# Performance work log

Measured on AMD Instinct MI355X. Metric: run time of the kernel, lower is better.

Reference implementation:

```python
import jax, jax.numpy as jnp
import numpy as np

NF, IN_NF, N_LAYERS = 64, 196, 3
B, H, W = 1, 256, 256
P3 = [(1, 1), (1, 1)]
P1 = [(0, 0), (0, 0)]


def conv2d(x, w, pad):
    return jax.lax.conv_general_dilated(x, w, (1, 1), pad,
                                        dimension_numbers=('NCHW', 'OIHW', 'NCHW'))


def prelu(x, a):
    return jnp.where(x >= 0, x, a[None, :, None, None] * x)


def warp(x, flow):
    # standard backward bilinear warp, zero padding outside the image
    Bx, C, Hx, Wx = x.shape
    yy, xx = jnp.meshgrid(jnp.arange(Hx, dtype=x.dtype),
                          jnp.arange(Wx, dtype=x.dtype), indexing='ij')
    px = xx[None] + flow[:, 0]  # (B,H,W)
    py = yy[None] + flow[:, 1]

    def sample(img, px, py):  # img (C,H,W); px,py (H,W)
        x0 = jnp.floor(px)
        y0 = jnp.floor(py)
        x1 = x0 + 1.0
        y1 = y0 + 1.0
        wx1 = px - x0
        wx0 = 1.0 - wx1
        wy1 = py - y0
        wy0 = 1.0 - wy1

        def gather(xi, yi):
            valid = (xi >= 0) & (xi <= Wx - 1) & (yi >= 0) & (yi <= Hx - 1)
            xc = jnp.clip(xi, 0, Wx - 1).astype(jnp.int32)
            yc = jnp.clip(yi, 0, Hx - 1).astype(jnp.int32)
            return img[:, yc, xc] * valid.astype(img.dtype)

        return (gather(x0, y0) * (wx0 * wy0) + gather(x1, y0) * (wx1 * wy0)
                + gather(x0, y1) * (wx0 * wy1) + gather(x1, y1) * (wx1 * wy1))

    return jax.vmap(sample)(x, px, py)


def setup_inputs() -> dict:
    key = jax.random.key(0)
    ks = jax.random.split(key, 11)
    s = 0.05
    return {
        'feat_0': jax.random.normal(ks[0], (B, 64, H, W), jnp.float32),
        'feat_1': jax.random.normal(ks[1], (B, 64, H, W), jnp.float32),
        'feat_dense': jax.random.normal(ks[2], (B, 64, H, W), jnp.float32),
        'flow': jax.random.normal(ks[3], (B, 4, H, W), jnp.float32),
        'space_mask': jax.random.uniform(ks[4], (B, 1, H, W), jnp.float32),
        'head_w': jax.random.normal(ks[5], (IN_NF, IN_NF, 3, 3), jnp.float32) * s,
        'head_a': jnp.full((IN_NF,), 0.25, jnp.float32),
        'conv_w': jax.random.normal(ks[6], (N_LAYERS, IN_NF, IN_NF, 3, 3), jnp.float32) * s,
        'conv_a': jnp.full((N_LAYERS, IN_NF), 0.25, jnp.float32),
        'last_w': jax.random.normal(ks[7], (4 + NF, IN_NF * (N_LAYERS + 1), 1, 1), jnp.float32) * s,
        'last_b': jax.random.normal(ks[8], (4 + NF,), jnp.float32) * s,
        'mask_w': jax.random.normal(ks[9], (2, NF, 3, 3), jnp.float32) * s,
        'mask_b': jax.random.normal(ks[10], (2,), jnp.float32) * s,
    }


def reference(feat_0, feat_1, feat_dense, flow, space_mask,
              head_w, head_a, conv_w, conv_a, last_w, last_b, mask_w, mask_b):
    f0 = warp(feat_0, flow[:, :2])
    f1 = warp(feat_1, flow[:, 2:4])
    x = jnp.concatenate([f0, f1, feat_dense, flow], axis=1)  # (B, in_nf, H, W)
    sm_up = jnp.repeat(jnp.repeat(space_mask, 2, axis=2), 2, axis=3)

    # head: conv3x3 -> PReLU, then mask (dense / use_sparsity=False path)
    x = prelu(conv2d(x, head_w, P3), head_a) * space_mask
    outs = [x]
    for i in range(N_LAYERS):
        x = conv2d(x, conv_w[i], P3) * space_mask
        x = prelu(x, conv_a[i])
        outs.append(x)
    x = conv2d(jnp.concatenate(outs, axis=1), last_w, P1) + last_b[None, :, None, None]

    smn = conv2d(x[:, 4:], mask_w, P3) + mask_b[None, :, None, None]

    Bx, Cx, Hx, Wx = x.shape
    x_up = jax.image.resize(x, (Bx, Cx, 2 * Hx, 2 * Wx), method='bilinear')
    smn_up = jax.image.resize(smn, (Bx, 2, 2 * Hx, 2 * Wx), method='bilinear')

    flow_out = x_up[:, :4]
    feat_t = x_up[:, 4:]
    # eval-mode mask (training=False): hard argmax between channel 0 and 1
    mask_next = (smn_up[:, :1] > smn_up[:, 1:2]).astype(x.dtype) * sm_up
    return flow_out, feat_t, mask_next
```

## Files before the change

kernel.cpp:

```cpp
#include <hip/hip_runtime.h>

typedef _Float16 f16;
typedef _Float16 f16x8 __attribute__((ext_vector_type(8)));
typedef _Float16 f16x4 __attribute__((ext_vector_type(4)));
typedef float    f32x4 __attribute__((ext_vector_type(4)));

#define MFMA16(a,b,c) __builtin_amdgcn_mfma_f32_16x16x32_f16(a,b,c,0,0,0)

#define NPIX 65536
#define CSTR 448
#define RB   (256*CSTR*2)
#define SBUF ((size_t)258*256*CSTR*2)

#define PK_OB   1024
#define PK_CB   14336
#define PK_TAP  100352
#define PK_CONV 903168
#define PKL_CB  5120
#define PKL_BI  35840

#define STG_BYTES 17408

__global__ void k_pack_conv(const float* __restrict__ head_w,
                            const float* __restrict__ conv_w,
                            f16* __restrict__ dst)
{
    int t = blockIdx.x*256 + threadIdx.x;
    if (t >= 4*9*7*14*2*64) return;
    int lane = t & 63; t >>= 6;
    int sel  = t & 1;  t >>= 1;
    int ob   = t % 14; t /= 14;
    int cb   = t % 7;  t /= 7;
    int tap  = t % 9;  t /= 9;
    int li   = t;
    const float* W = (li == 0) ? head_w : (conv_w + (size_t)(li-1)*196*196*9);
    int oc  = ob*16 + (lane & 15);
    int ic0 = cb*32 + (lane >> 4)*8;
    f16x8 v;
#pragma unroll
    for (int j = 0; j < 8; ++j) {
        int ic = ic0 + j;
        float x = 0.f;
        if (oc < 196 && ic < 196) x = W[((size_t)oc*196 + ic)*9 + tap];
        f16 h = (f16)x;
        v[j] = (sel == 0) ? h : (f16)(x - (float)h);
    }
    *(f16x8*)(dst + (size_t)li*PK_CONV +
              (((size_t)((tap*7+cb)*14 + ob)*2 + sel)*64 + lane)*8) = v;
}

__global__ void k_pack_last(const float* __restrict__ last_w, f16* __restrict__ dst)
{
    int t = blockIdx.x*256 + threadIdx.x;
    if (t >= 4*7*5*2*64) return;
    int lane = t & 63; t >>= 6;
    int sel  = t & 1;  t >>= 1;
    int ob   = t % 5;  t /= 5;
    int cb   = t % 7;  t /= 7;
    int bi   = t;
    int oc = ob*16 + (lane & 15);
    int k0 = cb*32 + (lane >> 4)*8;
    f16x8 v;
#pragma unroll
    for (int j = 0; j < 8; ++j) {
        int k = k0 + j;
        float x = 0.f;
        if (oc < 68 && k < 196) x = last_w[(size_t)oc*784 + bi*196 + k];
        f16 h = (f16)x;
        v[j] = (sel == 0) ? h : (f16)(x - (float)h);
    }
    *(f16x8*)(dst + (((size_t)((bi*7+cb)*5 + ob)*2 + sel)*64 + lane)*8) = v;
}

struct Gath { int o00,o01,o10,o11; float w00,w01,w10,w11; };

__device__ inline Gath mk_gath(float pxf, float pyf)
{
    float x0 = floorf(pxf), y0 = floorf(pyf);
    float x1 = x0 + 1.f, y1 = y0 + 1.f;
    float wx1 = pxf - x0, wx0 = 1.f - wx1;
    float wy1 = pyf - y0, wy0 = 1.f - wy1;
    bool vx0 = (x0 >= 0.f) && (x0 <= 255.f);
    bool vx1 = (x1 >= 0.f) && (x1 <= 255.f);
    bool vy0 = (y0 >= 0.f) && (y0 <= 255.f);
    bool vy1 = (y1 >= 0.f) && (y1 <= 255.f);
    int ix0 = min(max((int)x0, 0), 255);
    int ix1 = min(max((int)x1, 0), 255);
    int iy0 = min(max((int)y0, 0), 255);
    int iy1 = min(max((int)y1, 0), 255);
    Gath g;
    g.o00 = iy0*256 + ix0; g.w00 = (vx0 && vy0) ? wx0*wy0 : 0.f;
    g.o01 = iy0*256 + ix1; g.w01 = (vx1 && vy0) ? wx1*wy0 : 0.f;
    g.o10 = iy1*256 + ix0; g.w10 = (vx0 && vy1) ? wx0*wy1 : 0.f;
    g.o11 = iy1*256 + ix1; g.w11 = (vx1 && vy1) ? wx1*wy1 : 0.f;
    return g;
}

__device__ inline void store4(f16* __restrict__ op, int c0,
                              float a, float b, float c, float d)
{
    f16x4 hi, lo;
    f16 h;
    h = (f16)a; hi[0] = h; lo[0] = (f16)(a - (float)h);
    h = (f16)b; hi[1] = h; lo[1] = (f16)(b - (float)h);
    h = (f16)c; hi[2] = h; lo[2] = (f16)(c - (float)h);
    h = (f16)d; hi[3] = h; lo[3] = (f16)(d - (float)h);
    f16* p = op + (c0 >> 5)*64 + (c0 & 31);
    *(f16x4*)p        = hi;
    *(f16x4*)(p + 32) = lo;
}

__global__ void k_warp_concat(const float* __restrict__ f0, const float* __restrict__ f1,
                              const float* __restrict__ fd, const float* __restrict__ flow,
                              f16* __restrict__ out)
{
    int px = blockIdx.x*256 + threadIdx.x;
    int row = px >> 8, col = px & 255;
    f16* op = out + ((size_t)(row+1)*256 + col)*CSTR;
    Gath g0 = mk_gath((float)col + flow[px],          (float)row + flow[NPIX   + px]);
    Gath g1 = mk_gath((float)col + flow[2*NPIX + px], (float)row + flow[3*NPIX + px]);
#pragma unroll
    for (int c = 0; c < 64; c += 4) {
        float v[4];
#pragma unroll
        for (int r = 0; r < 4; ++r) {
            const float* im = f0 + (size_t)(c+r)*NPIX;
            v[r] = g0.w00*im[g0.o00] + g0.w01*im[g0.o01] + g0.w10*im[g0.o10] + g0.w11*im[g0.o11];
        }
        store4(op, c, v[0], v[1], v[2], v[3]);
    }
#pragma unroll
    for (int c = 0; c < 64; c += 4) {
        float v[4];
#pragma unroll
        for (int r = 0; r < 4; ++r) {
            const float* im = f1 + (size_t)(c+r)*NPIX;
            v[r] = g1.w00*im[g1.o00] + g1.w01*im[g1.o01] + g1.w10*im[g1.o10] + g1.w11*im[g1.o11];
        }
        store4(op, 64 + c, v[0], v[1], v[2], v[3]);
    }
#pragma unroll
    for (int c = 0; c < 64; c += 4) {
        store4(op, 128 + c, fd[(size_t)(c+0)*NPIX + px], fd[(size_t)(c+1)*NPIX + px],
                            fd[(size_t)(c+2)*NPIX + px], fd[(size_t)(c+3)*NPIX + px]);
    }
    store4(op, 192, flow[px], flow[NPIX+px], flow[2*NPIX+px], flow[3*NPIX+px]);
#pragma unroll
    for (int c = 196; c < 224; c += 4) store4(op, c, 0.f, 0.f, 0.f, 0.f);
}

__global__ __launch_bounds__(512, 4)
void k_conv3x3(const f16* __restrict__ in, f16* __restrict__ out,
               const f16* __restrict__ pack, const float* __restrict__ alpha,
               const float* __restrict__ mask, const f16* __restrict__ zp)
{
    __shared__ __align__(16) char bs[2*STG_BYTES];

    int bid = blockIdx.x;
    int wg  = (bid & 7)*64 + (bid >> 3);
    int row  = wg >> 1;
    int col0 = (wg & 1) << 7;

    int tid  = threadIdx.x;
    int lane = tid & 63;
    int w    = tid >> 6;
    int l15  = lane & 15, lk = lane >> 4;
    int och7   = (w & 1)*7;
    int pxbase = (w >> 1)*32;

    f32x4 acc[7][2];
#pragma unroll
    for (int o = 0; o < 7; ++o)
#pragma unroll
        for (int pb = 0; pb < 2; ++pb)
            acc[o][pb] = (f32x4){0.f,0.f,0.f,0.f};

    auto stage = [&](char* bufn, int ky, int cb) {
#pragma unroll
        for (int u = 0; u < 3; ++u) {
            int j = u*8 + w;
            if (j < 17) {
                int p  = j*8 + (lane >> 3);
                int sl = lane & 7;
                int cp = col0 - 1 + p;
                const f16* src;
                if (p < 130 && (unsigned)cp < 256u)
                    src = in + ((size_t)(row+ky)*256 + cp)*CSTR + cb*64 + ((sl ^ (p & 7)) * 8);
                else
                    src = zp + lane*8;
                __builtin_amdgcn_global_load_lds(
                    (const __attribute__((address_space(1))) void*)src,
                    (__attribute__((address_space(3))) void*)(bufn + j*1024),
                    16, 0, 0);
            }
        }
    };

    stage(bs, 0, 0);
    __syncthreads();

    for (int idx = 0; idx < 21; ++idx) {
        int ky = idx / 7;
        int cb = idx - ky*7;
        int nidx = idx + 1;
        if (nidx < 21) {
            int nky = nidx / 7;
            stage(bs + (nidx & 1)*STG_BYTES, nky, nidx - nky*7);
        }

        const char* bufc = bs + (idx & 1)*STG_BYTES;
        __builtin_amdgcn_s_setprio(1);
#pragma unroll
        for (int kx = 0; kx < 3; ++kx) {
            const f16* ap = pack + ((size_t)(((ky*3+kx)*7 + cb)*14 + och7))*1024 + (size_t)lane*8;
            f16x8 bh[2], bl[2];
#pragma unroll
            for (int pb = 0; pb < 2; ++pb) {
                int t = pxbase + pb*16 + l15 + kx;
                int sz = t & 7;
                const char* base = bufc + t*128;
                bh[pb] = *(const f16x8*)(base + ((lk ^ sz) << 4));
                bl[pb] = *(const f16x8*)(base + (((4+lk) ^ sz) << 4));
            }
#pragma unroll
            for (int o = 0; o < 7; ++o) {
                f16x8 ah = *(const f16x8*)(ap + o*1024);
                f16x8 al = *(const f16x8*)(ap + o*1024 + 512);
#pragma unroll
                for (int pb = 0; pb < 2; ++pb) {
                    acc[o][pb] = MFMA16(ah, bh[pb], acc[o][pb]);
                    acc[o][pb] = MFMA16(ah, bl[pb], acc[o][pb]);
                    acc[o][pb] = MFMA16(al, bh[pb], acc[o][pb]);
                }
            }
        }
        __builtin_amdgcn_s_setprio(0);
        __syncthreads();
    }

    float mv[2];
#pragma unroll
    for (int pb = 0; pb < 2; ++pb) mv[pb] = mask[row*256 + col0 + pxbase + pb*16 + l15];
#pragma unroll
    for (int o = 0; o < 7; ++o) {
        int oc0 = och7*16 + o*16 + lk*4;
        f32x4 a4 = *(const f32x4*)(alpha + min(oc0, 192));
#pragma unroll
        for (int pb = 0; pb < 2; ++pb) {
            f32x4 d = acc[o][pb];
            f16x4 hi, lo;
#pragma unroll
            for (int r = 0; r < 4; ++r) {
                float v = d[r];
                v = (v >= 0.f ? v : a4[r]*v) * mv[pb];
                f16 h = (f16)v;
                hi[r] = h;
                lo[r] = (f16)(v - (float)h);
            }
            f16* op = out + ((size_t)(row+1)*256 + col0 + pxbase + pb*16 + l15)*CSTR
                          + (oc0 >> 5)*64 + (oc0 & 31);
            *(f16x4*)op        = hi;
            *(f16x4*)(op + 32) = lo;
        }
    }
}

__global__ __launch_bounds__(256, 4)
void k_acc_last(const f16* __restrict__ in, const f16* __restrict__ pack,
                const float* __restrict__ bias, float* __restrict__ accp, int bi)
{
    int lane = threadIdx.x & 63;
    int wid  = (blockIdx.x << 2) | (threadIdx.x >> 6);
    int row  = wid >> 3;
    int col0 = (wid & 7) << 5;
    int l15 = lane & 15, lk = lane >> 4;

    f32x4 acc[5][2];
#pragma unroll
    for (int i = 0; i < 5; ++i)
#pragma unroll
        for (int j = 0; j < 2; ++j)
            acc[i][j] = (f32x4){0.f, 0.f, 0.f, 0.f};

    const f16* bb = in + ((size_t)(row+1)*256 + col0 + l15)*CSTR + lk*8;
    const f16* ap = pack + (size_t)bi*PKL_BI + (size_t)lane*8;
    for (int cb = 0; cb < 7; ++cb) {
        f16x8 bh[2], bl[2];
#pragma unroll
        for (int pb = 0; pb < 2; ++pb) {
            const f16* p = bb + (size_t)pb*(16*CSTR) + cb*64;
            bh[pb] = *(const f16x8*)p;
            bl[pb] = *(const f16x8*)(p + 32);
        }
        const f16* a = ap + cb*PKL_CB;
#pragma unroll
        for (int ob = 0; ob < 5; ++ob) {
            f16x8 ah = *(const f16x8*)(a + ob*1024);
            f16x8 al = *(const f16x8*)(a + ob*1024 + 512);
#pragma unroll
            for (int pb = 0; pb < 2; ++pb) {
                acc[ob][pb] = MFMA16(ah, bh[pb], acc[ob][pb]);
                acc[ob][pb] = MFMA16(ah, bl[pb], acc[ob][pb]);
                acc[ob][pb] = MFMA16(al, bh[pb], acc[ob][pb]);
            }
        }
    }
#pragma unroll
    for (int ob = 0; ob < 5; ++ob) {
        int oc0 = ob*16 + lk*4;
#pragma unroll
        for (int pb = 0; pb < 2; ++pb) {
            int px = row*256 + col0 + pb*16 + l15;
            float* dst = accp + (size_t)px*80 + oc0;
            f32x4 d = acc[ob][pb];
            if (bi == 0) {
                f32x4 b4;
#pragma unroll
                for (int r = 0; r < 4; ++r) b4[r] = bias[min(oc0 + r, 67)];
                *(f32x4*)dst = d + b4;
            } else {
                *(f32x4*)dst = *(const f32x4*)dst + d;
            }
        }
    }
}

__global__ void k_smn(const float* __restrict__ accp, const float* __restrict__ mw,
                      const float* __restrict__ mb, float* __restrict__ smn)
{
    int px = blockIdx.x*256 + threadIdx.x;
    int row = px >> 8, col = px & 255;
    float s0 = mb[0], s1 = mb[1];
    for (int ky = 0; ky < 3; ++ky) {
        int r = row + ky - 1;
        if ((unsigned)r > 255u) continue;
        for (int kx = 0; kx < 3; ++kx) {
            int c = col + kx - 1;
            if ((unsigned)c > 255u) continue;
            const float* ab = accp + ((size_t)r*256 + c)*80 + 4;
            const float* w  = mw + ky*3 + kx;
#pragma unroll
            for (int ch = 0; ch < 64; ch += 4) {
                f32x4 v = *(const f32x4*)(ab + ch);
                s0 += v[0]*w[(ch+0)*9] + v[1]*w[(ch+1)*9] + v[2]*w[(ch+2)*9] + v[3]*w[(ch+3)*9];
                s1 += v[0]*w[(64+ch+0)*9] + v[1]*w[(64+ch+1)*9] + v[2]*w[(64+ch+2)*9] + v[3]*w[(64+ch+3)*9];
            }
        }
    }
    smn[px]        = s0;
    smn[NPIX + px] = s1;
}

__global__ void k_upsample(const float* __restrict__ accp, float* __restrict__ outp)
{
    int o = blockIdx.x*256 + threadIdx.x;
    int oy = o >> 9, ox = o & 511;
    int my = oy >> 1, mx = ox >> 1;
    int r0, r1, c0, c1; float wy0, wy1, wx0, wx1;
    if (oy & 1) { r0 = my;            r1 = min(my+1, 255); wy0 = 0.75f; wy1 = 0.25f; }
    else        { r0 = max(my-1, 0);  r1 = my;             wy0 = 0.25f; wy1 = 0.75f; }
    if (ox & 1) { c0 = mx;            c1 = min(mx+1, 255); wx0 = 0.75f; wx1 = 0.25f; }
    else        { c0 = max(mx-1, 0);  c1 = mx;             wx0 = 0.25f; wx1 = 0.75f; }
    const float* p00 = accp + ((size_t)r0*256 + c0)*80;
    const float* p01 = accp + ((size_t)r0*256 + c1)*80;
    const float* p10 = accp + ((size_t)r1*256 + c0)*80;
    const float* p11 = accp + ((size_t)r1*256 + c1)*80;
    float w00 = wy0*wx0, w01 = wy0*wx1, w10 = wy1*wx0, w11 = wy1*wx1;
#pragma unroll
    for (int ch = 0; ch < 68; ch += 4) {
        f32x4 va = *(const f32x4*)(p00 + ch);
        f32x4 vb = *(const f32x4*)(p01 + ch);
        f32x4 vc = *(const f32x4*)(p10 + ch);
        f32x4 vd = *(const f32x4*)(p11 + ch);
        f32x4 v;
#pragma unroll
        for (int r = 0; r < 4; ++r)
            v[r] = w00*va[r] + w01*vb[r] + w10*vc[r] + w11*vd[r];
        outp[(size_t)(ch+0)*262144 + o] = v[0];
        outp[(size_t)(ch+1)*262144 + o] = v[1];
        outp[(size_t)(ch+2)*262144 + o] = v[2];
        outp[(size_t)(ch+3)*262144 + o] = v[3];
    }
}

__global__ void k_mask(const float* __restrict__ smn, const float* __restrict__ sm,
                       float* __restrict__ outp)
{
    int o = blockIdx.x*256 + threadIdx.x;
    int oy = o >> 9, ox = o & 511;
    int my = oy >> 1, mx = ox >> 1;
    int r0, r1, c0, c1; float wy0, wy1, wx0, wx1;
    if (oy & 1) { r0 = my;            r1 = min(my+1, 255); wy0 = 0.75f; wy1 = 0.25f; }
    else        { r0 = max(my-1, 0);  r1 = my;             wy0 = 0.25f; wy1 = 0.75f; }
    if (ox & 1) { c0 = mx;            c1 = min(mx+1, 255); wx0 = 0.75f; wx1 = 0.25f; }
    else        { c0 = max(mx-1, 0);  c1 = mx;             wx0 = 0.25f; wx1 = 0.75f; }
    float w00 = wy0*wx0, w01 = wy0*wx1, w10 = wy1*wx0, w11 = wy1*wx1;
    int i00 = r0*256 + c0, i01 = r0*256 + c1, i10 = r1*256 + c0, i11 = r1*256 + c1;
    float s0 = w00*smn[i00] + w01*smn[i01] + w10*smn[i10] + w11*smn[i11];
    float s1 = w00*smn[NPIX+i00] + w01*smn[NPIX+i01] + w10*smn[NPIX+i10] + w11*smn[NPIX+i11];
    outp[(size_t)68*262144 + o] = (s0 > s1) ? sm[my*256 + mx] : 0.f;
}

extern "C" void kernel_launch(void* const* d_in, const int* in_sizes, int n_in,
                              void* d_out, int out_size, void* d_ws, size_t ws_size,
                              hipStream_t stream)
{
    const float* feat0  = (const float*)d_in[0];
    const float* feat1  = (const float*)d_in[1];
    const float* featd  = (const float*)d_in[2];
    const float* flow   = (const float*)d_in[3];
    const float* smask  = (const float*)d_in[4];
    const float* head_w = (const float*)d_in[5];
    const float* head_a = (const float*)d_in[6];
    const float* conv_w = (const float*)d_in[7];
    const float* conv_a = (const float*)d_in[8];
    const float* last_w = (const float*)d_in[9];
    const float* last_b = (const float*)d_in[10];
    const float* mask_w = (const float*)d_in[11];
    const float* mask_b = (const float*)d_in[12];
    float* outp = (float*)d_out;

    char* ws = (char*)d_ws;
    size_t off = 0;
    f16* zp = (f16*)(ws + off); off += 4096;
    f16* bufA = (f16*)(ws + off); off += SBUF + 4096;
    f16* bufB = (f16*)(ws + off); off += SBUF + 4096;
    f16* packc = (f16*)(ws + off); off += (size_t)4*PK_CONV*2;
    f16* packl = (f16*)(ws + off); off += (size_t)4*PKL_BI*2;
    float* accp = (float*)(ws + off); off += (size_t)NPIX*80*4;
    float* smn  = (float*)(ws + off); off += (size_t)2*NPIX*4;

    hipMemsetAsync(zp, 0, 4096, stream);
    hipMemsetAsync(bufA, 0, RB, stream);
    hipMemsetAsync((char*)bufA + (size_t)257*RB, 0, RB, stream);
    hipMemsetAsync(bufB, 0, RB, stream);
    hipMemsetAsync((char*)bufB + (size_t)257*RB, 0, RB, stream);

    k_pack_conv<<<1764, 256, 0, stream>>>(head_w, conv_w, packc);
    k_pack_last<<<70, 256, 0, stream>>>(last_w, packl);
    k_warp_concat<<<256, 256, 0, stream>>>(feat0, feat1, featd, flow, bufA);

    k_conv3x3<<<512, 512, 0, stream>>>(bufA, bufB, packc, head_a, smask, zp);
    k_acc_last<<<512, 256, 0, stream>>>(bufB, packl, last_b, accp, 0);
    k_conv3x3<<<512, 512, 0, stream>>>(bufB, bufA, packc + (size_t)1*PK_CONV, conv_a, smask, zp);
    k_acc_last<<<512, 256, 0, stream>>>(bufA, packl, last_b, accp, 1);
    k_conv3x3<<<512, 512, 0, stream>>>(bufA, bufB, packc + (size_t)2*PK_CONV, conv_a + 196, smask, zp);
    k_acc_last<<<512, 256, 0, stream>>>(bufB, packl, last_b, accp, 2);
    k_conv3x3<<<512, 512, 0, stream>>>(bufB, bufA, packc + (size_t)3*PK_CONV, conv_a + 392, smask, zp);
    k_acc_last<<<512, 256, 0, stream>>>(bufA, packl, last_b, accp, 3);

    k_smn<<<256, 256, 0, stream>>>(accp, mask_w, mask_b, smn);
    k_upsample<<<1024, 256, 0, stream>>>(accp, outp);
    k_mask<<<1024, 256, 0, stream>>>(smn, smask, outp);
}
```

Baseline: 896.3 us.

## Switch 3x3 conv to 32x32 MFMA with K-blocked activation layout and no LDS

Activations move to a K-blocked layout (channel block, hi/lo half, 16-channel group, 8-channel half, pixel), with a zeroed halo column at each end of every row. The 3x3 conv kernel now uses 32x32x16 MFMA and reads operands straight from global memory, so the LDS double-buffer staging and its barriers are gone. Weight packing, warp_concat stores, acc_last loads and the accp stride (80 to 72) are all updated to match. The aim is fewer instructions per MFMA and no sync overhead, at the cost of relying on L1/L2 for reuse of the kx-shifted input.

```diff
diff --git a/kernel.cpp b/kernel.cpp
--- a/kernel.cpp
+++ b/kernel.cpp
@@ -4,38 +4,46 @@
 typedef _Float16 f16x8 __attribute__((ext_vector_type(8)));
 typedef _Float16 f16x4 __attribute__((ext_vector_type(4)));
 typedef float    f32x4 __attribute__((ext_vector_type(4)));
+typedef float    f32x16 __attribute__((ext_vector_type(16)));
 
 #define MFMA16(a,b,c) __builtin_amdgcn_mfma_f32_16x16x32_f16(a,b,c,0,0,0)
+#define MFMA32(a,b,c) __builtin_amdgcn_mfma_f32_32x32x16_f16(a,b,c,0,0,0)
 
 #define NPIX 65536
-#define CSTR 448
-#define RB   (256*CSTR*2)
-#define SBUF ((size_t)258*256*CSTR*2)
-
-#define PK_OB   1024
-#define PK_CB   14336
-#define PK_TAP  100352
+#define PXS   8
+#define KHS   2064
+#define K16S  4128
+#define HS    8256
+#define CBS   16512
+#define ROWH  115584
+#define RBYTES 231168
+#define SBUF  ((size_t)258*RBYTES)
+
+#define PKSTEP 7168
+#define PKCB   43008
 #define PK_CONV 903168
+
 #define PKL_CB  5120
 #define PKL_BI  35840
-
-#define STG_BYTES 17408
 
 __global__ void k_pack_conv(const float* __restrict__ head_w,
                             const float* __restrict__ conv_w,
                             f16* __restrict__ dst)
 {
     int t = blockIdx.x*256 + threadIdx.x;
-    if (t >= 4*9*7*14*2*64) return;
     int lane = t & 63; t >>= 6;
-    int sel  = t & 1;  t >>= 1;
-    int ob   = t % 14; t /= 14;
-    int cb   = t % 7;  t /= 7;
-    int tap  = t % 9;  t /= 9;
-    int li   = t;
+    int ob  = t % 7;  t /= 7;
+    int sel = t & 1;  t >>= 1;
+    int kx  = t % 3;  t /= 3;
+    int k16 = t & 1;  t >>= 1;
+    int cb  = t % 7;  t /= 7;
+    int ky  = t % 3;  t /= 3;
+    int li  = t;
+    if (li >= 4) return;
     const float* W = (li == 0) ? head_w : (conv_w + (size_t)(li-1)*196*196*9);
-    int oc  = ob*16 + (lane & 15);
-    int ic0 = cb*32 + (lane >> 4)*8;
+    int oc  = ob*32 + (lane & 31);
+    int ic0 = cb*32 + k16*16 + (lane >> 5)*8;
+    int tap = ky*3 + kx;
     f16x8 v;
 #pragma unroll
     for (int j = 0; j < 8; ++j) {
@@ -45,8 +53,8 @@
         f16 h = (f16)x;
         v[j] = (sel == 0) ? h : (f16)(x - (float)h);
     }
-    *(f16x8*)(dst + (size_t)li*PK_CONV +
-              (((size_t)((tap*7+cb)*14 + ob)*2 + sel)*64 + lane)*8) = v;
+    size_t frag = (((((size_t)(ky*7+cb)*2 + k16)*3 + kx)*2 + sel)*7 + ob);
+    *(f16x8*)(dst + (size_t)li*PK_CONV + frag*512 + (size_t)lane*8) = v;
 }
 
 __global__ void k_pack_last(const float* __restrict__ last_w, f16* __restrict__ dst)
@@ -70,6 +78,22 @@
         v[j] = (sel == 0) ? h : (f16)(x - (float)h);
     }
     *(f16x8*)(dst + (((size_t)((bi*7+cb)*5 + ob)*2 + sel)*64 + lane)*8) = v;
+}
+
+__global__ void k_zero_halo(f16* __restrict__ bufA, f16* __restrict__ bufB)
+{
+    int c = blockIdx.x*256 + threadIdx.x;
+    int end = c & 1; c >>= 1;
+    int kh  = c & 1; c >>= 1;
+    int k16 = c & 1; c >>= 1;
+    int h   = c & 1; c >>= 1;
+    int cb  = c % 7; c /= 7;
+    int row = c % 258; c /= 258;
+    if (c >= 2) return;
+    f16* base = (c == 0) ? bufA : bufB;
+    f16* p = base + (size_t)row*ROWH + cb*CBS + h*HS + k16*K16S + kh*KHS + (end ? 257 : 0)*PXS;
+    f16x8 z = {(f16)0,(f16)0,(f16)0,(f16)0,(f16)0,(f16)0,(f16)0,(f16)0};
+    *(f16x8*)p = z;
 }
 
 struct Gath { int o00,o01,o10,o11; float w00,w01,w10,w11; };
@@ -96,8 +120,8 @@
     return g;
 }
 
-__device__ inline void store4(f16* __restrict__ op, int c0,
-                              float a, float b, float c, float d)
+__device__ inline void store4n(f16* __restrict__ rowb, int slot, int c0,
+                               float a, float b, float c, float d)
 {
     f16x4 hi, lo;
     f16 h;
@@ -105,9 +129,11 @@
     h = (f16)b; hi[1] = h; lo[1] = (f16)(b - (float)h);
     h = (f16)c; hi[2] = h; lo[2] = (f16)(c - (float)h);
     h = (f16)d; hi[3] = h; lo[3] = (f16)(d - (float)h);
-    f16* p = op + (c0 >> 5)*64 + (c0 & 31);
+    int cb = c0 >> 5, w32 = c0 & 31;
+    f16* p = rowb + cb*CBS + (w32 >> 4)*K16S + ((w32 >> 3) & 1)*KHS
+                 + (size_t)slot*PXS + (w32 & 7);
     *(f16x4*)p        = hi;
-    *(f16x4*)(p + 32) = lo;
+    *(f16x4*)(p + HS) = lo;
 }
 
 __global__ void k_warp_concat(const float* __restrict__ f0, const float* __restrict__ f1,
@@ -116,7 +142,8 @@
 {
     int px = blockIdx.x*256 + threadIdx.x;
     int row = px >> 8, col = px & 255;
-    f16* op = out + ((size_t)(row+1)*256 + col)*CSTR;
+    f16* rowb = out + (size_t)(row+1)*ROWH;
+    int slot = col + 1;
     Gath g0 = mk_gath((float)col + flow[px],          (float)row + flow[NPIX   + px]);
     Gath g1 = mk_gath((float)col + flow[2*NPIX + px], (float)row + flow[3*NPIX + px]);
 #pragma unroll
@@ -127,7 +154,7 @@
             const float* im = f0 + (size_t)(c+r)*NPIX;
             v[r] = g0.w00*im[g0.o00] + g0.w01*im[g0.o01] + g0.w10*im[g0.o10] + g0.w11*im[g0.o11];
         }
-        store4(op, c, v[0], v[1], v[2], v[3]);
+        store4n(rowb, slot, c, v[0], v[1], v[2], v[3]);
     }
 #pragma unroll
     for (int c = 0; c < 64; c += 4) {
@@ -137,130 +164,91 @@
             const float* im = f1 + (size_t)(c+r)*NPIX;
             v[r] = g1.w00*im[g1.o00] + g1.w01*im[g1.o01] + g1.w10*im[g1.o10] + g1.w11*im[g1.o11];
         }
-        store4(op, 64 + c, v[0], v[1], v[2], v[3]);
+        store4n(rowb, slot, 64 + c, v[0], v[1], v[2], v[3]);
     }
 #pragma unroll
     for (int c = 0; c < 64; c += 4) {
-        store4(op, 128 + c, fd[(size_t)(c+0)*NPIX + px], fd[(size_t)(c+1)*NPIX + px],
-                            fd[(size_t)(c+2)*NPIX + px], fd[(size_t)(c+3)*NPIX + px]);
-    }
-    store4(op, 192, flow[px], flow[NPIX+px], flow[2*NPIX+px], flow[3*NPIX+px]);
-#pragma unroll
-    for (int c = 196; c < 224; c += 4) store4(op, c, 0.f, 0.f, 0.f, 0.f);
-}
-
-__global__ __launch_bounds__(512, 4)
-void k_conv3x3(const f16* __restrict__ in, f16* __restrict__ out,
-               const f16* __restrict__ pack, const float* __restrict__ alpha,
-               const float* __restrict__ mask, const f16* __restrict__ zp)
-{
-    __shared__ __align__(16) char bs[2*STG_BYTES];
-
+        store4n(rowb, slot, 128 + c, fd[(size_t)(c+0)*NPIX + px], fd[(size_t)(c+1)*NPIX + px],
+                                     fd[(size_t)(c+2)*NPIX + px], fd[(size_t)(c+3)*NPIX + px]);
+    }
+    store4n(rowb, slot, 192, flow[px], flow[NPIX+px], flow[2*NPIX+px], flow[3*NPIX+px]);
+#pragma unroll
+    for (int c = 196; c < 224; c += 4) store4n(rowb, slot, c, 0.f, 0.f, 0.f, 0.f);
+}
+
+__global__ __launch_bounds__(256, 2)
+void k_conv32(const f16* __restrict__ in, f16* __restrict__ out,
+              const f16* __restrict__ pack, const float* __restrict__ alpha,
+              const float* __restrict__ mask)
+{
     int bid = blockIdx.x;
     int wg  = (bid & 7)*64 + (bid >> 3);
     int row  = wg >> 1;
-    int col0 = (wg & 1) << 7;
-
-    int tid  = threadIdx.x;
-    int lane = tid & 63;
-    int w    = tid >> 6;
-    int l15  = lane & 15, lk = lane >> 4;
-    int och7   = (w & 1)*7;
-    int pxbase = (w >> 1)*32;
-
-    f32x4 acc[7][2];
+    int half = wg & 1;
+    int lane = threadIdx.x & 63;
+    int w    = threadIdx.x >> 6;
+    int pxt  = half*4 + w;
+    int l31 = lane & 31, lk = lane >> 5;
+
+    f32x16 acc[7];
 #pragma unroll
     for (int o = 0; o < 7; ++o)
 #pragma unroll
-        for (int pb = 0; pb < 2; ++pb)
-            acc[o][pb] = (f32x4){0.f,0.f,0.f,0.f};
-
-    auto stage = [&](char* bufn, int ky, int cb) {
-#pragma unroll
-        for (int u = 0; u < 3; ++u) {
-            int j = u*8 + w;
-            if (j < 17) {
-                int p  = j*8 + (lane >> 3);
-                int sl = lane & 7;
-                int cp = col0 - 1 + p;
-                const f16* src;
-                if (p < 130 && (unsigned)cp < 256u)
-                    src = in + ((size_t)(row+ky)*256 + cp)*CSTR + cb*64 + ((sl ^ (p & 7)) * 8);
-                else
-                    src = zp + lane*8;
-                __builtin_amdgcn_global_load_lds(
-                    (const __attribute__((address_space(1))) void*)src,
-                    (__attribute__((address_space(3))) void*)(bufn + j*1024),
-                    16, 0, 0);
-            }
-        }
-    };
-
-    stage(bs, 0, 0);
-    __syncthreads();
-
-    for (int idx = 0; idx < 21; ++idx) {
-        int ky = idx / 7;
-        int cb = idx - ky*7;
-        int nidx = idx + 1;
-        if (nidx < 21) {
-            int nky = nidx / 7;
-            stage(bs + (nidx & 1)*STG_BYTES, nky, nidx - nky*7);
-        }
-
-        const char* bufc = bs + (idx & 1)*STG_BYTES;
-        __builtin_amdgcn_s_setprio(1);
-#pragma unroll
-        for (int kx = 0; kx < 3; ++kx) {
-            const f16* ap = pack + ((size_t)(((ky*3+kx)*7 + cb)*14 + och7))*1024 + (size_t)lane*8;
-            f16x8 bh[2], bl[2];
-#pragma unroll
-            for (int pb = 0; pb < 2; ++pb) {
-                int t = pxbase + pb*16 + l15 + kx;
-                int sz = t & 7;
-                const char* base = bufc + t*128;
-                bh[pb] = *(const f16x8*)(base + ((lk ^ sz) << 4));
-                bl[pb] = *(const f16x8*)(base + (((4+lk) ^ sz) << 4));
-            }
-#pragma unroll
-            for (int o = 0; o < 7; ++o) {
-                f16x8 ah = *(const f16x8*)(ap + o*1024);
-                f16x8 al = *(const f16x8*)(ap + o*1024 + 512);
-#pragma unroll
-                for (int pb = 0; pb < 2; ++pb) {
-                    acc[o][pb] = MFMA16(ah, bh[pb], acc[o][pb]);
-                    acc[o][pb] = MFMA16(ah, bl[pb], acc[o][pb]);
-                    acc[o][pb] = MFMA16(al, bh[pb], acc[o][pb]);
+        for (int e = 0; e < 16; ++e) acc[o][e] = 0.f;
+
+    const f16* bcol = in + (size_t)lk*KHS + (size_t)(pxt*32 + l31)*PXS;
+    const f16* apl  = pack + (size_t)lane*8;
+
+    for (int ky = 0; ky < 3; ++ky) {
+        const f16* brow = bcol + (size_t)(row + ky)*ROWH;
+        for (int cb = 0; cb < 7; ++cb) {
+            const f16* bb  = brow + cb*CBS;
+            const f16* ap0 = apl + (size_t)(ky*7 + cb)*PKCB;
+#pragma unroll
+            for (int k16 = 0; k16 < 2; ++k16) {
+#pragma unroll
+                for (int kx = 0; kx < 3; ++kx) {
+                    const f16* bp = bb + k16*K16S + kx*PXS;
+                    f16x8 Bh = *(const f16x8*)bp;
+                    f16x8 Bl = *(const f16x8*)(bp + HS);
+                    const f16* ap = ap0 + (k16*3 + kx)*PKSTEP;
+                    f16x8 Ah[7], Al[7];
+#pragma unroll
+                    for (int o = 0; o < 7; ++o) {
+                        Ah[o] = *(const f16x8*)(ap + o*512);
+                        Al[o] = *(const f16x8*)(ap + 3584 + o*512);
+                    }
+#pragma unroll
+                    for (int o = 0; o < 7; ++o) acc[o] = MFMA32(Ah[o], Bh, acc[o]);
+#pragma unroll
+                    for (int o = 0; o < 7; ++o) acc[o] = MFMA32(Al[o], Bh, acc[o]);
+#pragma unroll
+                    for (int o = 0; o < 7; ++o) acc[o] = MFMA32(Ah[o], Bl, acc[o]);
                 }
             }
         }
-        __builtin_amdgcn_s_setprio(0);
-        __syncthreads();
-    }
-
-    float mv[2];
-#pragma unroll
-    for (int pb = 0; pb < 2; ++pb) mv[pb] = mask[row*256 + col0 + pxbase + pb*16 + l15];
+    }
+
+    float mv = mask[row*256 + pxt*32 + l31];
+    f16* orow = out + (size_t)(row+1)*ROWH + (size_t)(pxt*32 + l31 + 1)*PXS + lk*4;
 #pragma unroll
     for (int o = 0; o < 7; ++o) {
-        int oc0 = och7*16 + o*16 + lk*4;
-        f32x4 a4 = *(const f32x4*)(alpha + min(oc0, 192));
-#pragma unroll
-        for (int pb = 0; pb < 2; ++pb) {
-            f32x4 d = acc[o][pb];
+#pragma unroll
+        for (int qg = 0; qg < 4; ++qg) {
+            int oc0 = o*32 + 8*qg + 4*lk;
+            f32x4 a4 = *(const f32x4*)(alpha + min(oc0, 192));
             f16x4 hi, lo;
 #pragma unroll
-            for (int r = 0; r < 4; ++r) {
-                float v = d[r];
-                v = (v >= 0.f ? v : a4[r]*v) * mv[pb];
+            for (int e = 0; e < 4; ++e) {
+                float v = acc[o][qg*4 + e];
+                v = (v >= 0.f ? v : a4[e]*v) * mv;
                 f16 h = (f16)v;
-                hi[r] = h;
-                lo[r] = (f16)(v - (float)h);
+                hi[e] = h;
+                lo[e] = (f16)(v - (float)h);
             }
-            f16* op = out + ((size_t)(row+1)*256 + col0 + pxbase + pb*16 + l15)*CSTR
-                          + (oc0 >> 5)*64 + (oc0 & 31);
-            *(f16x4*)op        = hi;
-            *(f16x4*)(op + 32) = lo;
+            f16* p = orow + o*CBS + (qg >> 1)*K16S + (qg & 1)*KHS;
+            *(f16x4*)p        = hi;
+            *(f16x4*)(p + HS) = lo;
         }
     }
 }
@@ -282,15 +270,16 @@
         for (int j = 0; j < 2; ++j)
             acc[i][j] = (f32x4){0.f, 0.f, 0.f, 0.f};
 
-    const f16* bb = in + ((size_t)(row+1)*256 + col0 + l15)*CSTR + lk*8;
+    const f16* bb = in + (size_t)(row+1)*ROWH + (size_t)(col0 + l15 + 1)*PXS
+                  + (lk >> 1)*K16S + (lk & 1)*KHS;
     const f16* ap = pack + (size_t)bi*PKL_BI + (size_t)lane*8;
     for (int cb = 0; cb < 7; ++cb) {
         f16x8 bh[2], bl[2];
 #pragma unroll
         for (int pb = 0; pb < 2; ++pb) {
-            const f16* p = bb + (size_t)pb*(16*CSTR) + cb*64;
+            const f16* p = bb + cb*CBS + pb*16*PXS;
             bh[pb] = *(const f16x8*)p;
-            bl[pb] = *(const f16x8*)(p + 32);
+            bl[pb] = *(const f16x8*)(p + HS);
         }
         const f16* a = ap + cb*PKL_CB;
 #pragma unroll
@@ -308,10 +297,11 @@
 #pragma unroll
     for (int ob = 0; ob < 5; ++ob) {
         int oc0 = ob*16 + lk*4;
+        if (oc0 >= 72) continue;
 #pragma unroll
         for (int pb = 0; pb < 2; ++pb) {
             int px = row*256 + col0 + pb*16 + l15;
-            float* dst = accp + (size_t)px*80 + oc0;
+            float* dst = accp + (size_t)px*72 + oc0;
             f32x4 d = acc[ob][pb];
             if (bi == 0) {
                 f32x4 b4;
@@ -337,7 +327,7 @@
         for (int kx = 0; kx < 3; ++kx) {
             int c = col + kx - 1;
             if ((unsigned)c > 255u) continue;
-            const float* ab = accp + ((size_t)r*256 + c)*80 + 4;
+            const float* ab = accp + ((size_t)r*256 + c)*72 + 4;
             const float* w  = mw + ky*3 + kx;
 #pragma unroll
             for (int ch = 0; ch < 64; ch += 4) {
@@ -361,10 +351,10 @@
     else        { r0 = max(my-1, 0);  r1 = my;             wy0 = 0.25f; wy1 = 0.75f; }
     if (ox & 1) { c0 = mx;            c1 = min(mx+1, 255); wx0 = 0.75f; wx1 = 0.25f; }
     else        { c0 = max(mx-1, 0);  c1 = mx;             wx0 = 0.25f; wx1 = 0.75f; }
-    const float* p00 = accp + ((size_t)r0*256 + c0)*80;
-    const float* p01 = accp + ((size_t)r0*256 + c1)*80;
-    const float* p10 = accp + ((size_t)r1*256 + c0)*80;
-    const float* p11 = accp + ((size_t)r1*256 + c1)*80;
+    const float* p00 = accp + ((size_t)r0*256 + c0)*72;
+    const float* p01 = accp + ((size_t)r0*256 + c1)*72;
+    const float* p10 = accp + ((size_t)r1*256 + c0)*72;
+    const float* p11 = accp + ((size_t)r1*256 + c1)*72;
     float w00 = wy0*wx0, w01 = wy0*wx1, w10 = wy1*wx0, w11 = wy1*wx1;
 #pragma unroll
     for (int ch = 0; ch < 68; ch += 4) {
@@ -422,31 +412,30 @@
 
     char* ws = (char*)d_ws;
     size_t off = 0;
-    f16* zp = (f16*)(ws + off); off += 4096;
-    f16* bufA = (f16*)(ws + off); off += SBUF + 4096;
-    f16* bufB = (f16*)(ws + off); off += SBUF + 4096;
+    f16* bufA = (f16*)(ws + off); off += SBUF;
+    f16* bufB = (f16*)(ws + off); off += SBUF;
     f16* packc = (f16*)(ws + off); off += (size_t)4*PK_CONV*2;
     f16* packl = (f16*)(ws + off); off += (size_t)4*PKL_BI*2;
-    float* accp = (float*)(ws + off); off += (size_t)NPIX*80*4;
+    float* accp = (float*)(ws + off); off += (size_t)NPIX*72*4;
     float* smn  = (float*)(ws + off); off += (size_t)2*NPIX*4;
 
-    hipMemsetAsync(zp, 0, 4096, stream);
-    hipMemsetAsync(bufA, 0, RB, stream);
-    hipMemsetAsync((char*)bufA + (size_t)257*RB, 0, RB, stream);
-    hipMemsetAsync(bufB, 0, RB, stream);
-    hipMemsetAsync((char*)bufB + (size_t)257*RB, 0, RB, stream);
+    hipMemsetAsync(bufA, 0, RBYTES, stream);
+    hipMemsetAsync((char*)bufA + (size_t)257*RBYTES, 0, RBYTES, stream);
+    hipMemsetAsync(bufB, 0, RBYTES, stream);
+    hipMemsetAsync((char*)bufB + (size_t)257*RBYTES, 0, RBYTES, stream);
+    k_zero_halo<<<226, 256, 0, stream>>>(bufA, bufB);
 
     k_pack_conv<<<1764, 256, 0, stream>>>(head_w, conv_w, packc);
     k_pack_last<<<70, 256, 0, stream>>>(last_w, packl);
     k_warp_concat<<<256, 256, 0, stream>>>(feat0, feat1, featd, flow, bufA);
 
-    k_conv3x3<<<512, 512, 0, stream>>>(bufA, bufB, packc, head_a, smask, zp);
+    k_conv32<<<512, 256, 0, stream>>>(bufA, bufB, packc, head_a, smask);
     k_acc_last<<<512, 256, 0, stream>>>(bufB, packl, last_b, accp, 0);
-    k_conv3x3<<<512, 512, 0, stream>>>(bufB, bufA, packc + (size_t)1*PK_CONV, conv_a, smask, zp);
+    k_conv32<<<512, 256, 0, stream>>>(bufB, bufA, packc + (size_t)1*PK_CONV, conv_a, smask);
     k_acc_last<<<512, 256, 0, stream>>>(bufA, packl, last_b, accp, 1);
-    k_conv3x3<<<512, 512, 0, stream>>>(bufA, bufB, packc + (size_t)2*PK_CONV, conv_a + 196, smask, zp);
+    k_conv32<<<512, 256, 0, stream>>>(bufA, bufB, packc + (size_t)2*PK_CONV, conv_a + 196, smask);
     k_acc_last<<<512, 256, 0, stream>>>(bufB, packl, last_b, accp, 2);
-    k_conv3x3<<<512, 512, 0, stream>>>(bufB, bufA, packc + (size_t)3*PK_CONV, conv_a + 392, smask, zp);
+    k_conv32<<<512, 256, 0, stream>>>(bufB, bufA, packc + (size_t)3*PK_CONV, conv_a + 392, smask);
     k_acc_last<<<512, 256, 0, stream>>>(bufA, packl, last_b, accp, 3);
 
     k_smn<<<256, 256, 0, stream>>>(accp, mask_w, mask_b, smn);
```

Result: slower. 1.286 ms (+43.5%).
